# Performance work log

Hardware: AMD Instinct MI355X
Metric: run time of the kernel (lower is better)

Reference implementation:

```python
import jax, jax.numpy as jnp
import numpy as np


def setup_inputs() -> dict:
    key = jax.random.key(0)
    ks = jax.random.split(key, 16)
    B, S, D = 2, 2048, 1024
    H, SH, RH = 16, 1, 3
    hd = D // H
    w = 1.0 / np.sqrt(D)
    return {
        "x": jax.random.normal(ks[0], (B, S, D), jnp.float32),
        "Wq": jax.random.normal(ks[1], (D, D), jnp.float32) * w,
        "bq": jnp.zeros((D,), jnp.float32),
        "Wk": jax.random.normal(ks[2], (D, D), jnp.float32) * w,
        "bk": jnp.zeros((D,), jnp.float32),
        "Wv": jax.random.normal(ks[3], (D, D), jnp.float32) * w,
        "bv": jnp.zeros((D,), jnp.float32),
        "Wproj": jax.random.normal(ks[4], (D, D), jnp.float32) * w,
        "bproj": jnp.zeros((D,), jnp.float32),
        "Wr": jax.random.normal(ks[5], (D, H - SH), jnp.float32) * w,
        "br": jnp.zeros((H - SH,), jnp.float32),
        "Ws": jax.random.normal(ks[6], (D, 2), jnp.float32) * w,
        "bs": jnp.zeros((2,), jnp.float32),
        "temperature": jnp.zeros((H, 1, 1), jnp.float32),
        "query_embedding": jax.random.truncated_normal(ks[7], -2.0, 2.0, (H, 1, hd), jnp.float32) * 0.02,
        "num_heads": H,
        "shared_heads": SH,
        "routed_heads": RH,
    }


def reference(x, Wq, bq, Wk, bk, Wv, bv, Wproj, bproj, Wr, br, Ws, bs,
              temperature, query_embedding, num_heads, shared_heads, routed_heads):
    B, S, D = x.shape
    H = num_heads
    hd = D // H

    def split_heads(t):  # [B,S,D] -> [B,H,S,hd]
        return t.reshape(B, S, H, hd).transpose(0, 2, 1, 3)

    q = split_heads(x @ Wq + bq)
    k = split_heads(x @ Wk + bk)
    v = split_heads(x @ Wv + bv)

    # L2-normalize q along head_dim, add learned query embedding, scale by softplus(temperature)
    q_norm = q * jax.lax.rsqrt(jnp.sum(q * q, axis=-1, keepdims=True) + 1e-12)
    q_scaled = (q_norm + query_embedding[None]) * jax.nn.softplus(temperature)[None]

    attn = jnp.einsum('bhqd,bhkd->bhqk', q_scaled, k) / jnp.sqrt(jnp.float32(hd))
    attn = jax.nn.softmax(attn, axis=-1)
    o = jnp.einsum('bhqk,bhkd->bhqd', attn, v)
    o = o.transpose(0, 2, 1, 3).reshape(B, S, D)  # [B,S,D]

    # Routed-head gating via top-k router
    gates = jax.nn.softmax(o @ Wr + br, axis=-1)          # [B,S,H-SH]
    _, idx = jax.lax.top_k(gates, routed_heads)           # [B,S,RH]
    mask = jax.nn.one_hot(idx, H - shared_heads, dtype=gates.dtype).sum(axis=2)
    routed_gates = gates * mask * jnp.float32(routed_heads)

    # Shared-head gating
    sw = jax.nn.softmax(o @ Ws + bs, axis=-1)             # [B,S,2]
    shared_gates = sw * jnp.float32(shared_heads)
    w0 = sw * 2.0
    shared_gates = w0[..., 0:1] * shared_gates
    routed_gates = w0[..., 1:2] * routed_gates
    masked_gates = jnp.concatenate([shared_gates, routed_gates], axis=-1)

    # einsum('bnh,bnd->bnd') sums over h: scales o by sum of gates
    o = masked_gates.sum(axis=-1, keepdims=True) * o
    return o @ Wproj + bproj
```

## Files before the change

### kernel.cpp

```cpp
#include <hip/hip_runtime.h>
#include <hip/hip_bf16.h>

typedef unsigned short ushort_t;
typedef unsigned int uint_t;

typedef __attribute__((ext_vector_type(8))) short bf8;
typedef __attribute__((ext_vector_type(4))) float f4;
typedef __attribute__((ext_vector_type(16))) float f16v;

__device__ __forceinline__ float bf2f(ushort_t u) {
    unsigned int x = ((unsigned int)u) << 16;
    return __uint_as_float(x);
}
__device__ __forceinline__ ushort_t f2bf(float f) {
    unsigned int x = __float_as_uint(f);
    unsigned int r = x + 0x7fffu + ((x >> 16) & 1u);
    return (ushort_t)(r >> 16);
}
__device__ __forceinline__ uint_t pack2bf(float a, float b) {
    return (uint_t)f2bf(a) | ((uint_t)f2bf(b) << 16);
}
__device__ __forceinline__ uint_t pack2bf_fast(float a, float b) {
    uint_t au = __float_as_uint(a) + 0x8000u;
    uint_t bu = __float_as_uint(b) + 0x8000u;
    return __builtin_amdgcn_perm(bu, au, 0x07060302);
}

__device__ __forceinline__ void gl2lds16(const ushort_t* g, ushort_t* l) {
    __builtin_amdgcn_global_load_lds(
        (const __attribute__((address_space(1))) void*)g,
        (__attribute__((address_space(3))) void*)l, 16, 0, 0);
}

__global__ __launch_bounds__(256)
void prep(const float* __restrict__ x, ushort_t* __restrict__ xb,
          const float* __restrict__ Wr, const float* __restrict__ Ws,
          ushort_t* __restrict__ Wg,
          const float* __restrict__ W0, const float* __restrict__ W1,
          const float* __restrict__ W2, const float* __restrict__ W3,
          ushort_t* __restrict__ T0, ushort_t* __restrict__ T1,
          ushort_t* __restrict__ T2, ushort_t* __restrict__ T3)
{
    __shared__ float tile[32][33];
    int bid = blockIdx.x;
    int t = threadIdx.x;
    if (bid < 4096) {
        int i = bid * 256 + t;
        float4 v = ((const float4*)x)[i];
        uint2 o;
        o.x = pack2bf(v.x, v.y);
        o.y = pack2bf(v.z, v.w);
        ((uint2*)xb)[i] = o;
    } else if (bid < 4224) {
        int idx = (bid - 4096) * 256 + t;
        int c = idx >> 10, d = idx & 1023;
        float v = 0.f;
        if (c < 15) v = Wr[(size_t)d * 15 + c];
        else if (c < 17) v = Ws[(size_t)d * 2 + (c - 15)];
        Wg[idx] = f2bf(v);
    } else {
        int idx = bid - 4224;
        int z = idx >> 10, r10 = idx & 1023;
        int k0 = (r10 & 31) * 32, n0 = (r10 >> 5) * 32;
        const float* W; ushort_t* T;
        switch (z) {
            case 0: W = W0; T = T0; break;
            case 1: W = W1; T = T1; break;
            case 2: W = W2; T = T2; break;
            default: W = W3; T = T3; break;
        }
        int r = t >> 3, c4 = (t & 7) * 4;
        float4 v = *(const float4*)&W[(size_t)(k0 + r) * 1024 + n0 + c4];
        tile[r][c4 + 0] = v.x; tile[r][c4 + 1] = v.y;
        tile[r][c4 + 2] = v.z; tile[r][c4 + 3] = v.w;
        __syncthreads();
        int n = t >> 3, kk = (t & 7) * 4;
        uint2 o;
        o.x = pack2bf(tile[kk][n], tile[kk + 1][n]);
        o.y = pack2bf(tile[kk + 2][n], tile[kk + 3][n]);
        *(uint2*)&T[(size_t)(n0 + n) * 1024 + k0 + kk] = o;
    }
}

__global__ __launch_bounds__(256)
void gemmQKV(const ushort_t* __restrict__ A, const ushort_t* __restrict__ Wt3,
             const float* __restrict__ bq, const float* __restrict__ bk,
             const float* __restrict__ bv,
             ushort_t* __restrict__ Qb, ushort_t* __restrict__ Kw,
             ushort_t* __restrict__ VTw,
             const float* __restrict__ temp, const float* __restrict__ emb)
{
    const int K = 1024;
    __shared__ ushort_t As[128 * 64];
    __shared__ ushort_t Bs[128 * 64];

    int t = threadIdx.x;
    int m0 = blockIdx.x * 128;
    int y = blockIdx.y;
    int region = y >> 3;
    int n0 = (y & 7) * 128;

    int lane = t & 63, w = t >> 6;
    int lm = lane & 15, quad = lane >> 4;
    int wm = (w >> 1) * 64, wn = (w & 1) * 64;

    f4 acc[4][4] = {};

    int srow = t >> 3;
    int schunk = ((t & 7) ^ (srow & 7)) * 8;
    const ushort_t* pA = &A[(size_t)(m0 + srow) * K + schunk];
    const ushort_t* pB = &Wt3[(size_t)(y * 128 + srow) * K + schunk];
    const size_t rstep = (size_t)32 * K;

    for (int k0 = 0; k0 < K; k0 += 64) {
        #pragma unroll
        for (int j = 0; j < 4; j++) {
            gl2lds16(pA + j * rstep, &As[(t + j * 256) * 8]);
            gl2lds16(pB + j * rstep, &Bs[(t + j * 256) * 8]);
        }
        pA += 64; pB += 64;
        __syncthreads();

        #pragma unroll
        for (int ks = 0; ks < 2; ks++) {
            int rc = ((ks * 4 + quad) ^ (lm & 7)) * 8;
            bf8 af[4], bfr[4];
            #pragma unroll
            for (int mi = 0; mi < 4; mi++)
                af[mi] = *(bf8*)&As[(wm + mi * 16 + lm) * 64 + rc];
            #pragma unroll
            for (int ni = 0; ni < 4; ni++)
                bfr[ni] = *(bf8*)&Bs[(wn + ni * 16 + lm) * 64 + rc];
            if (region == 2) {
                #pragma unroll
                for (int mi = 0; mi < 4; mi++)
                #pragma unroll
                for (int ni = 0; ni < 4; ni++)
                    acc[mi][ni] = __builtin_amdgcn_mfma_f32_16x16x32_bf16(af[mi], bfr[ni], acc[mi][ni], 0, 0, 0);
            } else {
                #pragma unroll
                for (int ni = 0; ni < 4; ni++)
                #pragma unroll
                for (int mi = 0; mi < 4; mi++)
                    acc[ni][mi] = __builtin_amdgcn_mfma_f32_16x16x32_bf16(bfr[ni], af[mi], acc[ni][mi], 0, 0, 0);
            }
        }
        __syncthreads();
    }

    if (region == 0) {
        int head = (n0 + wn) >> 6;
        float sp = log1pf(__expf(temp[head]));
        f4 bv4[4], ev4[4];
        #pragma unroll
        for (int ni = 0; ni < 4; ni++) {
            bv4[ni] = *(const f4*)&bq[n0 + wn + ni * 16 + quad * 4];
            ev4[ni] = *(const f4*)&emb[head * 64 + ni * 16 + quad * 4];
        }
        #pragma unroll
        for (int mi = 0; mi < 4; mi++) {
            float v[4][4];
            float ss = 0.f;
            #pragma unroll
            for (int ni = 0; ni < 4; ni++)
            #pragma unroll
            for (int i = 0; i < 4; i++) {
                v[ni][i] = acc[ni][mi][i] + bv4[ni][i];
                ss += v[ni][i] * v[ni][i];
            }
            ss += __shfl_xor(ss, 16, 64);
            ss += __shfl_xor(ss, 32, 64);
            float rs = rsqrtf(ss + 1e-12f);
            int tok = m0 + wm + mi * 16 + lm;
            int b = tok >> 11, s = tok & 2047;
            size_t rowb = (((size_t)(b * 16 + head)) * 2048 + s) * 64;
            #pragma unroll
            for (int ni = 0; ni < 4; ni++) {
                uint2 o;
                o.x = pack2bf((v[ni][0] * rs + ev4[ni][0]) * sp * 0.125f,
                              (v[ni][1] * rs + ev4[ni][1]) * sp * 0.125f);
                o.y = pack2bf((v[ni][2] * rs + ev4[ni][2]) * sp * 0.125f,
                              (v[ni][3] * rs + ev4[ni][3]) * sp * 0.125f);
                *(uint2*)&Qb[rowb + ni * 16 + quad * 4] = o;
            }
        }
    } else if (region == 1) {
        int head = (n0 + wn) >> 6;
        f4 bv4[4];
        #pragma unroll
        for (int ni = 0; ni < 4; ni++)
            bv4[ni] = *(const f4*)&bk[n0 + wn + ni * 16 + quad * 4];
        #pragma unroll
        for (int mi = 0; mi < 4; mi++) {
            int tok = m0 + wm + mi * 16 + lm;
            int b = tok >> 11, s = tok & 2047;
            size_t rowb = (((size_t)(b * 16 + head)) * 2048 + s) * 64;
            #pragma unroll
            for (int ni = 0; ni < 4; ni++) {
                uint2 o;
                o.x = pack2bf(acc[ni][mi][0] + bv4[ni][0], acc[ni][mi][1] + bv4[ni][1]);
                o.y = pack2bf(acc[ni][mi][2] + bv4[ni][2], acc[ni][mi][3] + bv4[ni][3]);
                *(uint2*)&Kw[rowb + ni * 16 + quad * 4] = o;
            }
        }
    } else {
        float bvv[4];
        #pragma unroll
        for (int ni = 0; ni < 4; ni++) bvv[ni] = bv[n0 + wn + ni * 16 + lm];
        #pragma unroll
        for (int mi = 0; mi < 4; mi++) {
            int gr0 = m0 + wm + mi * 16 + quad * 4;
            int b = gr0 >> 11, s0 = gr0 & 2047;
            #pragma unroll
            for (int ni = 0; ni < 4; ni++) {
                int gc = n0 + wn + ni * 16 + lm;
                int h = gc >> 6, d = gc & 63;
                uint2 o;
                o.x = pack2bf(acc[mi][ni][0] + bvv[ni], acc[mi][ni][1] + bvv[ni]);
                o.y = pack2bf(acc[mi][ni][2] + bvv[ni], acc[mi][ni][3] + bvv[ni]);
                *(uint2*)&VTw[(((size_t)(b * 16 + h)) * 64 + d) * 2048 + s0] = o;
            }
        }
    }
}

__global__ __launch_bounds__(256)
void gemmP(const ushort_t* __restrict__ A, const ushort_t* __restrict__ Wt,
           const float* __restrict__ bias, const float* __restrict__ G,
           float* __restrict__ out, int M, int N, int K)
{
    __shared__ ushort_t As[128 * 64];
    __shared__ ushort_t Bs[128 * 64];

    int t = threadIdx.x;
    int m0 = blockIdx.x * 128, n0 = blockIdx.y * 128;
    int lane = t & 63, w = t >> 6;
    int lm = lane & 15, quad = lane >> 4;
    int wm = (w >> 1) * 64, wn = (w & 1) * 64;

    f4 acc[4][4] = {};

    int srow = t >> 3;
    int schunk = ((t & 7) ^ (srow & 7)) * 8;
    const ushort_t* pA = &A[(size_t)(m0 + srow) * K + schunk];
    const ushort_t* pB = &Wt[(size_t)(n0 + srow) * K + schunk];
    const size_t rstep = (size_t)32 * K;

    for (int k0 = 0; k0 < K; k0 += 64) {
        #pragma unroll
        for (int j = 0; j < 4; j++) {
            gl2lds16(pA + j * rstep, &As[(t + j * 256) * 8]);
            gl2lds16(pB + j * rstep, &Bs[(t + j * 256) * 8]);
        }
        pA += 64; pB += 64;
        __syncthreads();

        #pragma unroll
        for (int ks = 0; ks < 2; ks++) {
            int rc = ((ks * 4 + quad) ^ (lm & 7)) * 8;
            bf8 af[4], bfr[4];
            #pragma unroll
            for (int mi = 0; mi < 4; mi++)
                af[mi] = *(bf8*)&As[(wm + mi * 16 + lm) * 64 + rc];
            #pragma unroll
            for (int ni = 0; ni < 4; ni++)
                bfr[ni] = *(bf8*)&Bs[(wn + ni * 16 + lm) * 64 + rc];
            #pragma unroll
            for (int ni = 0; ni < 4; ni++)
            #pragma unroll
            for (int mi = 0; mi < 4; mi++)
                acc[ni][mi] = __builtin_amdgcn_mfma_f32_16x16x32_bf16(bfr[ni], af[mi], acc[ni][mi], 0, 0, 0);
        }
        __syncthreads();
    }

    f4 bv4[4];
    #pragma unroll
    for (int ni = 0; ni < 4; ni++)
        bv4[ni] = *(const f4*)&bias[n0 + wn + ni * 16 + quad * 4];
    #pragma unroll
    for (int mi = 0; mi < 4; mi++) {
        int tok = m0 + wm + mi * 16 + lm;
        float g = G[tok];
        size_t rowb = (size_t)tok * N + n0 + wn;
        #pragma unroll
        for (int ni = 0; ni < 4; ni++) {
            f4 o;
            #pragma unroll
            for (int i = 0; i < 4; i++) o[i] = g * acc[ni][mi][i] + bv4[ni][i];
            *(f4*)&out[rowb + ni * 16 + quad * 4] = o;
        }
    }
}

__global__ __launch_bounds__(256)
void attn(const ushort_t* __restrict__ Q, const ushort_t* __restrict__ K,
          const ushort_t* __restrict__ VT, ushort_t* __restrict__ Opart,
          float* __restrict__ Lw)
{
    __shared__ ushort_t Ks[64 * 72];
    __shared__ ushort_t Vt[64 * 72];

    int t = threadIdx.x, lane = t & 63, w = t >> 6;
    int l31 = lane & 31;
    uint_t hi = lane >> 5;
    int bid = blockIdx.x;
    int bh = bid & 31, qt = (bid >> 5) & 15, ks = bid >> 9;
    size_t base = (size_t)bh * 2048 * 64;

    int tok = qt * 128 + w * 32 + l31;
    const ushort_t* qp = &Q[base + (size_t)tok * 64 + hi * 8];
    bf8 qa[4];
    #pragma unroll
    for (int c = 0; c < 4; c++) qa[c] = *(const bf8*)(qp + c * 16);

    float l_part = 0.f;
    f16v o_acc[2] = {};

    int sr = t >> 3, sc = (t & 7) * 8;
    const ushort_t* kg0 = &K[base + (size_t)sr * 64 + sc];
    const ushort_t* vg0 = &VT[base + (size_t)sr * 2048 + sc];

    int kend = ks * 1024 + 1024;
    for (int kb = ks * 1024; kb < kend; kb += 64) {
        __syncthreads();
        {
            uint4 k0 = *(const uint4*)(kg0 + (size_t)kb * 64);
            uint4 k1 = *(const uint4*)(kg0 + (size_t)(kb + 32) * 64);
            uint4 v0 = *(const uint4*)(vg0 + kb);
            uint4 v1 = *(const uint4*)(vg0 + 32 * 2048 + kb);
            *(uint4*)&Ks[sr * 72 + sc] = k0;
            *(uint4*)&Ks[(sr + 32) * 72 + sc] = k1;
            *(uint4*)&Vt[sr * 72 + sc] = v0;
            *(uint4*)&Vt[(sr + 32) * 72 + sc] = v1;
        }
        __syncthreads();

        bf8 pf[4];
        #pragma unroll
        for (int kt2 = 0; kt2 < 2; kt2++) {
            f16v s = {};
            #pragma unroll
            for (int c = 0; c < 4; c++) {
                bf8 kf = *(bf8*)&Ks[(kt2 * 32 + l31) * 72 + c * 16 + hi * 8];
                s = __builtin_amdgcn_mfma_f32_32x32x16_bf16(kf, qa[c], s, 0, 0, 0);
            }
            uint2 pk[4];
            #pragma unroll
            for (int g = 0; g < 4; g++) {
                float p0 = __expf(s[g * 4 + 0]);
                float p1 = __expf(s[g * 4 + 1]);
                float p2 = __expf(s[g * 4 + 2]);
                float p3 = __expf(s[g * 4 + 3]);
                l_part += (p0 + p1) + (p2 + p3);
                pk[g].x = pack2bf_fast(p0, p1);
                pk[g].y = pack2bf_fast(p2, p3);
            }
            #pragma unroll
            for (int cc = 0; cc < 2; cc++) {
                uint_t sx = hi ? pk[2 * cc].x : pk[2 * cc + 1].x;
                uint_t sy = hi ? pk[2 * cc].y : pk[2 * cc + 1].y;
                uint_t rx = (uint_t)__shfl_xor((int)sx, 32, 64);
                uint_t ry = (uint_t)__shfl_xor((int)sy, 32, 64);
                uint4 u;
                u.x = hi ? rx : pk[2 * cc].x;
                u.y = hi ? ry : pk[2 * cc].y;
                u.z = hi ? pk[2 * cc + 1].x : rx;
                u.w = hi ? pk[2 * cc + 1].y : ry;
                pf[kt2 * 2 + cc] = *(bf8*)&u;
            }
        }

        #pragma unroll
        for (int c = 0; c < 4; c++) {
            #pragma unroll
            for (int dt = 0; dt < 2; dt++) {
                bf8 vf = *(bf8*)&Vt[(dt * 32 + l31) * 72 + c * 16 + hi * 8];
                o_acc[dt] = __builtin_amdgcn_mfma_f32_32x32x16_bf16(vf, pf[c], o_acc[dt], 0, 0, 0);
            }
        }
    }

    l_part += __shfl_xor(l_part, 32, 64);
    if (hi == 0) Lw[((size_t)ks * 32 + bh) * 2048 + tok] = l_part;

    size_t pbase = (((size_t)(ks * 32 + bh)) * 2048 + tok) * 64;
    #pragma unroll
    for (int dt = 0; dt < 2; dt++)
    #pragma unroll
    for (int g = 0; g < 4; g++) {
        int d0 = dt * 32 + g * 8 + hi * 4;
        uint2 o;
        o.x = pack2bf_fast(o_acc[dt][g * 4 + 0], o_acc[dt][g * 4 + 1]);
        o.y = pack2bf_fast(o_acc[dt][g * 4 + 2], o_acc[dt][g * 4 + 3]);
        *(uint2*)&Opart[pbase + d0] = o;
    }
}

__global__ __launch_bounds__(256)
void combine(const ushort_t* __restrict__ Opart, const float* __restrict__ Lw,
             ushort_t* __restrict__ Ob)
{
    int i = blockIdx.x * 256 + threadIdx.x;
    int flat = i * 4;
    int row = flat >> 6;
    int d = flat & 63;
    int bh = row >> 11, tok = row & 2047;
    int b = bh >> 4, h = bh & 15;
    float rl = 1.f / (Lw[row] + Lw[65536 + row]);
    uint2 p0 = *(const uint2*)&Opart[flat];
    uint2 p1 = *(const uint2*)&Opart[4194304 + flat];
    float v0 = (bf2f(p0.x & 0xffff) + bf2f(p1.x & 0xffff)) * rl;
    float v1 = (bf2f(p0.x >> 16)   + bf2f(p1.x >> 16))   * rl;
    float v2 = (bf2f(p0.y & 0xffff) + bf2f(p1.y & 0xffff)) * rl;
    float v3 = (bf2f(p0.y >> 16)   + bf2f(p1.y >> 16))   * rl;
    uint2 o;
    o.x = pack2bf(v0, v1);
    o.y = pack2bf(v2, v3);
    *(uint2*)&Ob[((size_t)(b * 2048 + tok)) * 1024 + h * 64 + d] = o;
}

__global__ __launch_bounds__(256)
void router(const ushort_t* __restrict__ O, const ushort_t* __restrict__ Wg,
            const float* __restrict__ br, const float* __restrict__ bs,
            float* __restrict__ G)
{
    __shared__ float Ls[64][21];
    int t = threadIdx.x, lane = t & 63, w = t >> 6;
    int lm = lane & 15, quad = lane >> 4;
    int tok0 = blockIdx.x * 64;

    const ushort_t* ap = &O[(size_t)(tok0 + w * 16 + lm) * 1024 + quad * 8];
    const ushort_t* b0p = &Wg[(size_t)lm * 1024 + quad * 8];
    const ushort_t* b1p = &Wg[(size_t)(16 + lm) * 1024 + quad * 8];

    f4 acc0 = {}, acc1 = {};
    for (int k0 = 0; k0 < 1024; k0 += 32) {
        bf8 a = *(const bf8*)(ap + k0);
        bf8 b0 = *(const bf8*)(b0p + k0);
        bf8 b1 = *(const bf8*)(b1p + k0);
        acc0 = __builtin_amdgcn_mfma_f32_16x16x32_bf16(a, b0, acc0, 0, 0, 0);
        acc1 = __builtin_amdgcn_mfma_f32_16x16x32_bf16(a, b1, acc1, 0, 0, 0);
    }
    #pragma unroll
    for (int i = 0; i < 4; i++) {
        int tl = w * 16 + quad * 4 + i;
        Ls[tl][lm] = acc0[i];
        if (lm == 0) Ls[tl][16] = acc1[i];
    }
    __syncthreads();
    if (t < 64) {
        float v[15];
        float mx = -1e30f;
        #pragma unroll
        for (int c = 0; c < 15; c++) { v[c] = Ls[t][c] + br[c]; mx = fmaxf(mx, v[c]); }
        float sum = 0.f;
        #pragma unroll
        for (int c = 0; c < 15; c++) { v[c] = __expf(v[c] - mx); sum += v[c]; }
        float inv = 1.f / sum;
        float t3 = 0.f;
        for (int r = 0; r < 3; r++) {
            int bi = 0; float bv = -1e30f;
            #pragma unroll
            for (int c = 0; c < 15; c++) if (v[c] > bv) { bv = v[c]; bi = c; }
            t3 += bv; v[bi] = -1e30f;
        }
        t3 *= inv;
        float a0 = Ls[t][15] + bs[0], a1 = Ls[t][16] + bs[1];
        float m2 = fmaxf(a0, a1);
        float e0 = __expf(a0 - m2), e1 = __expf(a1 - m2);
        G[tok0 + t] = (2.f * e0 + 6.f * e1 * t3) / (e0 + e1);
    }
}

extern "C" void kernel_launch(void* const* d_in, const int* in_sizes, int n_in,
                              void* d_out, int out_size, void* d_ws, size_t ws_size,
                              hipStream_t stream)
{
    const float* x     = (const float*)d_in[0];
    const float* Wq    = (const float*)d_in[1];
    const float* bq    = (const float*)d_in[2];
    const float* Wk    = (const float*)d_in[3];
    const float* bk    = (const float*)d_in[4];
    const float* Wv    = (const float*)d_in[5];
    const float* bv    = (const float*)d_in[6];
    const float* Wproj = (const float*)d_in[7];
    const float* bproj = (const float*)d_in[8];
    const float* Wr    = (const float*)d_in[9];
    const float* br    = (const float*)d_in[10];
    const float* Ws    = (const float*)d_in[11];
    const float* bs    = (const float*)d_in[12];
    const float* temp  = (const float*)d_in[13];
    const float* emb   = (const float*)d_in[14];

    const int M = 4096, N = 1024, Kd = 1024;

    char* ws = (char*)d_ws;
    ushort_t* Kw    = (ushort_t*)ws;
    ushort_t* VTw   = (ushort_t*)(ws + 8388608);
    ushort_t* Qb    = (ushort_t*)(ws + 16777216);
    ushort_t* Wtp   = (ushort_t*)(ws + 25165824);
    float*    Gw    = (float*)(ws + 27262976);
    ushort_t* Wg    = (ushort_t*)(ws + 27279360);
    float*    Lw    = (float*)(ws + 27344896);
    ushort_t* Wt3   = (ushort_t*)(ws + 27869184);
    ushort_t* xb    = (ushort_t*)(ws + 34160640);
    ushort_t* Opart = (ushort_t*)(ws + 27869184);
    ushort_t* Ob    = Qb;

    prep<<<8320, 256, 0, stream>>>(x, xb, Wr, Ws, Wg, Wq, Wk, Wv, Wproj,
        Wt3, Wt3 + 1048576, Wt3 + 2097152, Wtp);

    gemmQKV<<<dim3(32, 24), 256, 0, stream>>>(xb, Wt3, bq, bk, bv,
        Qb, Kw, VTw, temp, emb);

    attn<<<1024, 256, 0, stream>>>(Qb, Kw, VTw, Opart, Lw);

    combine<<<4096, 256, 0, stream>>>(Opart, Lw, Ob);

    router<<<64, 256, 0, stream>>>(Ob, Wg, br, bs, Gw);

    gemmP<<<dim3(32, 8), 256, 0, stream>>>(Ob, Wtp, bproj, Gw, (float*)d_out, M, N, Kd);
}
```

Before: 252.3 us.

## Prefetch K/V tiles into registers and use native exp2, pack, and permlane ops

The attention loop now loads the next K/V tile into registers while the current tile is computed, replacing the load-sync-compute pattern with register double buffering plus a trailing barrier. The log2(e) factor is folded into the Q scaling so softmax can use raw v_exp_f32. bf16 packing now uses v_cvt_pk_bf16_f32, and the cross-half lane exchange uses v_permlane32_swap instead of a shuffle with selects. The extra register pressure may lower occupancy. The last iteration's prefetch reads one tile past the valid range, which can run past the end of the buffer.

```diff
diff --git a/kernel.cpp b/kernel.cpp
--- a/kernel.cpp
+++ b/kernel.cpp
@@ -24,6 +24,15 @@
     uint_t au = __float_as_uint(a) + 0x8000u;
     uint_t bu = __float_as_uint(b) + 0x8000u;
     return __builtin_amdgcn_perm(bu, au, 0x07060302);
+}
+__device__ __forceinline__ float exp2_fast(float x) {
+    float r; asm("v_exp_f32 %0, %1" : "=v"(r) : "v"(x)); return r;
+}
+__device__ __forceinline__ uint_t cvtpk_bf16(float lo, float hi) {
+    uint_t r; asm("v_cvt_pk_bf16_f32 %0, %1, %2" : "=v"(r) : "v"(lo), "v"(hi)); return r;
+}
+__device__ __forceinline__ void pl32swap(uint_t &a, uint_t &b) {
+    asm("v_permlane32_swap_b32 %0, %1" : "+v"(a), "+v"(b));
 }
 
 __device__ __forceinline__ void gl2lds16(const ushort_t* g, ushort_t* l) {
@@ -151,6 +160,7 @@
     if (region == 0) {
         int head = (n0 + wn) >> 6;
         float sp = log1pf(__expf(temp[head]));
+        float qs = sp * 0.18033688011112042f;
         f4 bv4[4], ev4[4];
         #pragma unroll
         for (int ni = 0; ni < 4; ni++) {
@@ -177,10 +187,10 @@
             #pragma unroll
             for (int ni = 0; ni < 4; ni++) {
                 uint2 o;
-                o.x = pack2bf((v[ni][0] * rs + ev4[ni][0]) * sp * 0.125f,
-                              (v[ni][1] * rs + ev4[ni][1]) * sp * 0.125f);
-                o.y = pack2bf((v[ni][2] * rs + ev4[ni][2]) * sp * 0.125f,
-                              (v[ni][3] * rs + ev4[ni][3]) * sp * 0.125f);
+                o.x = pack2bf((v[ni][0] * rs + ev4[ni][0]) * qs,
+                              (v[ni][1] * rs + ev4[ni][1]) * qs);
+                o.y = pack2bf((v[ni][2] * rs + ev4[ni][2]) * qs,
+                              (v[ni][3] * rs + ev4[ni][3]) * qs);
                 *(uint2*)&Qb[rowb + ni * 16 + quad * 4] = o;
             }
         }
@@ -318,23 +328,27 @@
     f16v o_acc[2] = {};
 
     int sr = t >> 3, sc = (t & 7) * 8;
-    const ushort_t* kg0 = &K[base + (size_t)sr * 64 + sc];
-    const ushort_t* vg0 = &VT[base + (size_t)sr * 2048 + sc];
-
-    int kend = ks * 1024 + 1024;
-    for (int kb = ks * 1024; kb < kend; kb += 64) {
-        __syncthreads();
-        {
-            uint4 k0 = *(const uint4*)(kg0 + (size_t)kb * 64);
-            uint4 k1 = *(const uint4*)(kg0 + (size_t)(kb + 32) * 64);
-            uint4 v0 = *(const uint4*)(vg0 + kb);
-            uint4 v1 = *(const uint4*)(vg0 + 32 * 2048 + kb);
-            *(uint4*)&Ks[sr * 72 + sc] = k0;
-            *(uint4*)&Ks[(sr + 32) * 72 + sc] = k1;
-            *(uint4*)&Vt[sr * 72 + sc] = v0;
-            *(uint4*)&Vt[(sr + 32) * 72 + sc] = v1;
-        }
-        __syncthreads();
+    const ushort_t* kp = &K[base + (size_t)(ks * 1024 + sr) * 64 + sc];
+    const ushort_t* vp = &VT[base + (size_t)sr * 2048 + ks * 1024 + sc];
+
+    uint4 rk0 = *(const uint4*)(kp);
+    uint4 rk1 = *(const uint4*)(kp + 32 * 64);
+    uint4 rv0 = *(const uint4*)(vp);
+    uint4 rv1 = *(const uint4*)(vp + 32 * 2048);
+    kp += 64 * 64; vp += 64;
+
+    for (int it = 0; it < 16; ++it) {
+        *(uint4*)&Ks[sr * 72 + sc] = rk0;
+        *(uint4*)&Ks[(sr + 32) * 72 + sc] = rk1;
+        *(uint4*)&Vt[sr * 72 + sc] = rv0;
+        *(uint4*)&Vt[(sr + 32) * 72 + sc] = rv1;
+        __syncthreads();
+
+        rk0 = *(const uint4*)(kp);
+        rk1 = *(const uint4*)(kp + 32 * 64);
+        rv0 = *(const uint4*)(vp);
+        rv1 = *(const uint4*)(vp + 32 * 2048);
+        kp += 64 * 64; vp += 64;
 
         bf8 pf[4];
         #pragma unroll
@@ -345,28 +359,25 @@
                 bf8 kf = *(bf8*)&Ks[(kt2 * 32 + l31) * 72 + c * 16 + hi * 8];
                 s = __builtin_amdgcn_mfma_f32_32x32x16_bf16(kf, qa[c], s, 0, 0, 0);
             }
-            uint2 pk[4];
+            uint_t px[4], py[4];
             #pragma unroll
             for (int g = 0; g < 4; g++) {
-                float p0 = __expf(s[g * 4 + 0]);
-                float p1 = __expf(s[g * 4 + 1]);
-                float p2 = __expf(s[g * 4 + 2]);
-                float p3 = __expf(s[g * 4 + 3]);
+                float p0 = exp2_fast(s[g * 4 + 0]);
+                float p1 = exp2_fast(s[g * 4 + 1]);
+                float p2 = exp2_fast(s[g * 4 + 2]);
+                float p3 = exp2_fast(s[g * 4 + 3]);
                 l_part += (p0 + p1) + (p2 + p3);
-                pk[g].x = pack2bf_fast(p0, p1);
-                pk[g].y = pack2bf_fast(p2, p3);
+                px[g] = cvtpk_bf16(p0, p1);
+                py[g] = cvtpk_bf16(p2, p3);
             }
             #pragma unroll
             for (int cc = 0; cc < 2; cc++) {
-                uint_t sx = hi ? pk[2 * cc].x : pk[2 * cc + 1].x;
-                uint_t sy = hi ? pk[2 * cc].y : pk[2 * cc + 1].y;
-                uint_t rx = (uint_t)__shfl_xor((int)sx, 32, 64);
-                uint_t ry = (uint_t)__shfl_xor((int)sy, 32, 64);
+                uint_t ax = px[2 * cc], bx = px[2 * cc + 1];
+                uint_t ay = py[2 * cc], by = py[2 * cc + 1];
+                pl32swap(ax, bx);
+                pl32swap(ay, by);
                 uint4 u;
-                u.x = hi ? rx : pk[2 * cc].x;
-                u.y = hi ? ry : pk[2 * cc].y;
-                u.z = hi ? pk[2 * cc + 1].x : rx;
-                u.w = hi ? pk[2 * cc + 1].y : ry;
+                u.x = ax; u.y = ay; u.z = bx; u.w = by;
                 pf[kt2 * 2 + cc] = *(bf8*)&u;
             }
         }
@@ -379,6 +390,7 @@
                 o_acc[dt] = __builtin_amdgcn_mfma_f32_32x32x16_bf16(vf, pf[c], o_acc[dt], 0, 0, 0);
             }
         }
+        __syncthreads();
     }
 
     l_part += __shfl_xor(l_part, 32, 64);
```

Result: faster. 245.2 us (-2.8%).
